# Kernel optimization log

Measured on AMD Instinct MI355X. Metric: run time of the kernel, lower is better.

## Reference

```python
import jax, jax.numpy as jnp
import numpy as np

B, T, I, H = 64, 1024, 256, 512

def setup_inputs() -> dict:
    key = jax.random.key(0)
    ks = jax.random.split(key, 16)
    stdv = 1.0 / np.sqrt(H)
    u = lambda k, shp: jax.random.uniform(k, shp, jnp.float32, -stdv, stdv)
    inp = {"x": jax.random.normal(ks[0], (B, T, I), jnp.float32)}
    names = ["i", "f", "h", "o"]
    for n, g in enumerate(names):
        inp[f"U_{g}"] = u(ks[1 + 3 * n], (I, H))
        inp[f"V_{g}"] = u(ks[2 + 3 * n], (H, H))
        inp[f"b_{g}"] = u(ks[3 + 3 * n], (H,))
    inp["fc_w"] = u(ks[13], (1, H))
    inp["fc_b"] = u(ks[14], (1,))
    return inp

def _lstm_last_h(x, U_i, V_i, b_i, U_f, V_f, b_f, U_h, V_h, b_h, U_o, V_o, b_o):
    # Precompute input projections for all timesteps: [T, B, 4H]
    U = jnp.concatenate([U_i, U_f, U_h, U_o], axis=1)          # [I, 4H]
    b = jnp.concatenate([b_i, b_f, b_h, b_o], axis=0)          # [4H]
    V = jnp.concatenate([V_i, V_f, V_h, V_o], axis=1)          # [H, 4H]
    xproj = jnp.einsum("bti,ig->tbg", x, U) + b                # [T, B, 4H]
    Hn = U_i.shape[1]

    def step(carry, xp_t):
        h, c = carry
        gates = xp_t + h @ V                                   # [B, 4H]
        i_t = jax.nn.sigmoid(gates[:, 0 * Hn:1 * Hn])
        f_t = jax.nn.sigmoid(gates[:, 1 * Hn:2 * Hn])
        g_t = jnp.tanh(gates[:, 2 * Hn:3 * Hn])
        o_t = jax.nn.sigmoid(gates[:, 3 * Hn:4 * Hn])
        c = f_t * c + i_t * g_t
        h = o_t * jnp.tanh(c)
        return (h, c), None

    h0 = jnp.zeros((x.shape[0], Hn), x.dtype)
    c0 = jnp.zeros((x.shape[0], Hn), x.dtype)
    (h_last, _), _ = jax.lax.scan(step, (h0, c0), xproj)
    return h_last

def reference(x, U_i, V_i, b_i, U_f, V_f, b_f, U_h, V_h, b_h, U_o, V_o, b_o, fc_w, fc_b):
    h_last = _lstm_last_h(x, U_i, V_i, b_i, U_f, V_f, b_f, U_h, V_h, b_h, U_o, V_o, b_o)
    return h_last @ fc_w.T + fc_b                              # [B, 1]
```

## Files before the change

kernel.cpp:

```cpp
#include <hip/hip_runtime.h>

typedef _Float16 h8 __attribute__((ext_vector_type(8)));
typedef float    f4 __attribute__((ext_vector_type(4)));
typedef unsigned u4 __attribute__((ext_vector_type(4)));

static const unsigned long long WS_NEEDED = 262144ull;

__device__ __forceinline__ float sigm(float x)   { return 1.0f / (1.0f + __expf(-x)); }
__device__ __forceinline__ float tanh_a(float x) { return 2.0f / (1.0f + __expf(-2.0f * x)) - 1.0f; }

__global__ __launch_bounds__(256) void k_init(unsigned* hbuf)
{
    const int idx = blockIdx.x * 256 + threadIdx.x;
    if (idx < 65536) hbuf[idx] = 0x000003FFu;
}


#define VWAIT0() do { asm volatile("s_waitcnt vmcnt(0)" ::: "memory"); \
                      __builtin_amdgcn_sched_barrier(0); } while (0)
#define LBAR()   do { asm volatile("s_waitcnt lgkmcnt(0)" ::: "memory"); \
                      __builtin_amdgcn_s_barrier(); \
                      __builtin_amdgcn_sched_barrier(0); } while (0)

#define PROBE4() \
    asm volatile( \
        "global_load_dwordx4 %0, %4, off sc0 sc1\n\t" \
        "global_load_dwordx4 %1, %4, off offset:16 sc0 sc1\n\t" \
        "global_load_dwordx4 %2, %4, off offset:1024 sc0 sc1\n\t" \
        "global_load_dwordx4 %3, %4, off offset:1040 sc0 sc1" \
        : "=&v"(qa), "=&v"(qb), "=&v"(qc), "=&v"(qd) \
        : "v"(hp) : "memory")

__device__ __forceinline__ h8 pack8h(u4 a, u4 b)
{
    h8 p;
    p[0] = (_Float16)__uint_as_float(a[0] & 0xFFFFFC00u);
    p[1] = (_Float16)__uint_as_float(a[1] & 0xFFFFFC00u);
    p[2] = (_Float16)__uint_as_float(a[2] & 0xFFFFFC00u);
    p[3] = (_Float16)__uint_as_float(a[3] & 0xFFFFFC00u);
    p[4] = (_Float16)__uint_as_float(b[0] & 0xFFFFFC00u);
    p[5] = (_Float16)__uint_as_float(b[1] & 0xFFFFFC00u);
    p[6] = (_Float16)__uint_as_float(b[2] & 0xFFFFFC00u);
    p[7] = (_Float16)__uint_as_float(b[3] & 0xFFFFFC00u);
    return p;
}
__device__ __forceinline__ h8 pack8f(f4 a, f4 b)
{
    h8 p;
    p[0] = (_Float16)a[0]; p[1] = (_Float16)a[1];
    p[2] = (_Float16)a[2]; p[3] = (_Float16)a[3];
    p[4] = (_Float16)b[0]; p[5] = (_Float16)b[1];
    p[6] = (_Float16)b[2]; p[7] = (_Float16)b[3];
    return p;
}

__global__ __launch_bounds__(256, 1) void k_rec(
    const float* __restrict__ x,
    const float* __restrict__ Ui, const float* __restrict__ Vi, const float* __restrict__ bi,
    const float* __restrict__ Uf, const float* __restrict__ Vf, const float* __restrict__ bf,
    const float* __restrict__ Uh, const float* __restrict__ Vh, const float* __restrict__ bh,
    const float* __restrict__ Uo, const float* __restrict__ Vo, const float* __restrict__ bo,
    unsigned* hbuf)
{
    const int bx = blockIdx.x;
    const int ig = bx & 7;
    const int jg = bx >> 3;
    const int tid = threadIdx.x;
    const int w = tid >> 6, l = tid & 63;
    const int lo = l & 15, hi = l >> 4;
    const int r8 = lo & 7;
    const int unit = jg * 64 + w * 16 + lo;

    __shared__ __align__(16) _Float16 ldsH[2][16 * 32 * 8];
    __shared__ __align__(16) _Float16 ldsX[2][8 * 32 * 8];

    const float* Ug[4] = {Ui, Uf, Uh, Uo};
    const float* Vg[4] = {Vi, Vf, Vh, Vo};
    const float* bg[4] = {bi, bf, bh, bo};

    h8 vfrag[4][16];
    h8 ufrag[4][8];
    float bias[4];
#pragma unroll
    for (int g = 0; g < 4; ++g) {
        bias[g] = bg[g][unit];
#pragma unroll
        for (int kc = 0; kc < 16; ++kc) {
            h8 v;
#pragma unroll
            for (int jj = 0; jj < 8; ++jj)
                v[jj] = (_Float16)Vg[g][(size_t)(kc * 32 + hi * 8 + jj) * 512 + unit];
            vfrag[g][kc] = v;
        }
#pragma unroll
        for (int kc = 0; kc < 8; ++kc) {
            h8 u;
#pragma unroll
            for (int jj = 0; jj < 8; ++jj)
                u[jj] = (_Float16)Ug[g][(size_t)(kc * 32 + hi * 8 + jj) * 512 + unit];
            ufrag[g][kc] = u;
        }
    }

    const int sr = tid >> 5;
    const int sc = (tid & 31) * 8;
    const int kc1 = sc >> 5;
    const int hg1 = (sc >> 3) & 3;
    const int sw1 = ((kc1 & 1) << 2) | hg1;
    const int g1 = kc1 * 32 + hg1 * 8 + (sr ^ sw1);
    const int g2 = (kc1 + 8) * 32 + hg1 * 8 + (sr ^ sw1);

    const float* xrb = x + (size_t)(ig * 8 + sr) * 262144 + sc;

    f4 cst = {0.f, 0.f, 0.f, 0.f};
    f4 xq0, xq1;

    {
        f4 a0, a1;
        asm volatile("global_load_dwordx4 %0, %2, off\n\t"
                     "global_load_dwordx4 %1, %2, off offset:16"
                     : "=&v"(a0), "=&v"(a1) : "v"(xrb) : "memory");
        VWAIT0();
        *(h8*)&ldsX[0][(size_t)g1 * 8] = pack8f(a0, a1);
        const float* xp1 = xrb + 256;
        asm volatile("global_load_dwordx4 %0, %2, off\n\t"
                     "global_load_dwordx4 %1, %2, off offset:16"
                     : "=&v"(xq0), "=&v"(xq1) : "v"(xp1) : "memory");
        LBAR();
    }

    for (int t = 0; t < 1024; ++t) {
        const int pb = t & 1, pn = pb ^ 1;
        const int pr = (t + 1) & 1;
        const unsigned etag = (unsigned)((t + 1023) & 1023);
        const unsigned* hp = hbuf + (size_t)(pr * 8 + ig) * 4096
                                  + (size_t)sr * 512 + sc;

        f4 acc[4], acq[4];
#pragma unroll
        for (int g = 0; g < 4; ++g) {
            f4 a; a[0] = bias[g]; a[1] = bias[g]; a[2] = bias[g]; a[3] = bias[g];
            acc[g] = a;
            f4 z; z[0] = 0.f; z[1] = 0.f; z[2] = 0.f; z[3] = 0.f;
            acq[g] = z;
        }
#pragma unroll
        for (int k = 0; k < 4; ++k) {
            const int ke = 2 * k, ko = 2 * k + 1;
            const int ga = ke * 32 + hi * 8 + (r8 ^ (((ke & 1) << 2) | hi));
            const int gb = ko * 32 + hi * 8 + (r8 ^ (((ko & 1) << 2) | hi));
            const h8 xa = *(const h8*)&ldsX[pb][(size_t)ga * 8];
            const h8 xb = *(const h8*)&ldsX[pb][(size_t)gb * 8];
            acc[0] = __builtin_amdgcn_mfma_f32_16x16x32_f16(xa, ufrag[0][ke], acc[0], 0, 0, 0);
            acc[1] = __builtin_amdgcn_mfma_f32_16x16x32_f16(xa, ufrag[1][ke], acc[1], 0, 0, 0);
            acc[2] = __builtin_amdgcn_mfma_f32_16x16x32_f16(xa, ufrag[2][ke], acc[2], 0, 0, 0);
            acc[3] = __builtin_amdgcn_mfma_f32_16x16x32_f16(xa, ufrag[3][ke], acc[3], 0, 0, 0);
            acq[0] = __builtin_amdgcn_mfma_f32_16x16x32_f16(xb, ufrag[0][ko], acq[0], 0, 0, 0);
            acq[1] = __builtin_amdgcn_mfma_f32_16x16x32_f16(xb, ufrag[1][ko], acq[1], 0, 0, 0);
            acq[2] = __builtin_amdgcn_mfma_f32_16x16x32_f16(xb, ufrag[2][ko], acq[2], 0, 0, 0);
            acq[3] = __builtin_amdgcn_mfma_f32_16x16x32_f16(xb, ufrag[3][ko], acq[3], 0, 0, 0);
        }

        u4 qa, qb, qc, qd;
        PROBE4();

        {
            int tries = 0;
            for (;;) {
                VWAIT0();
                const unsigned m =
                    (qa[0]^etag)|(qa[1]^etag)|(qa[2]^etag)|(qa[3]^etag)|
                    (qb[0]^etag)|(qb[1]^etag)|(qb[2]^etag)|(qb[3]^etag)|
                    (qc[0]^etag)|(qc[1]^etag)|(qc[2]^etag)|(qc[3]^etag)|
                    (qd[0]^etag)|(qd[1]^etag)|(qd[2]^etag)|(qd[3]^etag);
                if (__all((m & 1023u) == 0u)) break;
                if (++tries > 8192) break;
                PROBE4();
            }
        }

        *(h8*)&ldsX[pn][(size_t)g1 * 8] = pack8f(xq0, xq1);
        *(h8*)&ldsH[pb][(size_t)g1 * 8] = pack8h(qa, qb);
        *(h8*)&ldsH[pb][(size_t)g2 * 8] = pack8h(qc, qd);

        {
            const int tn = (t + 2 < 1024) ? t + 2 : 1023;
            const float* xp = xrb + (size_t)tn * 256;
            asm volatile("global_load_dwordx4 %0, %2, off\n\t"
                         "global_load_dwordx4 %1, %2, off offset:16"
                         : "=&v"(xq0), "=&v"(xq1) : "v"(xp) : "memory");
        }

        LBAR();

#pragma unroll
        for (int k = 0; k < 8; ++k) {
            const int kh = k + 8;
            const int ga = k  * 32 + hi * 8 + (r8 ^ (((k  & 1) << 2) | hi));
            const int gb = kh * 32 + hi * 8 + (r8 ^ (((kh & 1) << 2) | hi));
            const h8 a0 = *(const h8*)&ldsH[pb][(size_t)ga * 8];
            const h8 a1 = *(const h8*)&ldsH[pb][(size_t)gb * 8];
            acc[0] = __builtin_amdgcn_mfma_f32_16x16x32_f16(a0, vfrag[0][k],  acc[0], 0, 0, 0);
            acc[1] = __builtin_amdgcn_mfma_f32_16x16x32_f16(a0, vfrag[1][k],  acc[1], 0, 0, 0);
            acc[2] = __builtin_amdgcn_mfma_f32_16x16x32_f16(a0, vfrag[2][k],  acc[2], 0, 0, 0);
            acc[3] = __builtin_amdgcn_mfma_f32_16x16x32_f16(a0, vfrag[3][k],  acc[3], 0, 0, 0);
            acq[0] = __builtin_amdgcn_mfma_f32_16x16x32_f16(a1, vfrag[0][kh], acq[0], 0, 0, 0);
            acq[1] = __builtin_amdgcn_mfma_f32_16x16x32_f16(a1, vfrag[1][kh], acq[1], 0, 0, 0);
            acq[2] = __builtin_amdgcn_mfma_f32_16x16x32_f16(a1, vfrag[2][kh], acq[2], 0, 0, 0);
            acq[3] = __builtin_amdgcn_mfma_f32_16x16x32_f16(a1, vfrag[3][kh], acq[3], 0, 0, 0);
        }

        const unsigned ptag = (unsigned)(t & 1023);
        unsigned pub[4];
#pragma unroll
        for (int d = 0; d < 4; ++d) {
            const float iv = sigm(acc[0][d] + acq[0][d]);
            const float fv = sigm(acc[1][d] + acq[1][d]);
            const float gv = tanh_a(acc[2][d] + acq[2][d]);
            const float ov = sigm(acc[3][d] + acq[3][d]);
            const float c = fv * cst[d] + iv * gv;
            cst[d] = c;
            const float hv = ov * tanh_a(c);
            pub[d] = (__float_as_uint(hv) & 0xFFFFFC00u) | ptag;
        }
        if (hi < 2) {
            unsigned* hw = hbuf + (size_t)((pb * 8 + ig) * 8 + hi * 4) * 512 + unit;
            asm volatile(
                "global_store_dword %4, %0, off sc0 sc1\n\t"
                "global_store_dword %4, %1, off offset:2048 sc0 sc1\n\t"
                "global_store_dword %5, %2, off sc0 sc1\n\t"
                "global_store_dword %5, %3, off offset:2048 sc0 sc1"
                :: "v"(pub[0]), "v"(pub[1]), "v"(pub[2]), "v"(pub[3]),
                   "v"(hw), "v"(hw + 1024)
                : "memory");
        }
    }
}

__global__ __launch_bounds__(64) void k_fc(
    const unsigned* __restrict__ hbuf, const float* __restrict__ fcw,
    const float* __restrict__ fcb, float* __restrict__ out)
{
    const int b = blockIdx.x, l = threadIdx.x;
    const unsigned* h = hbuf + (size_t)((8 + (b >> 3)) * 8 + (b & 7)) * 512;
    float s = 0.f;
#pragma unroll
    for (int k = 0; k < 8; ++k) {
        const float hv = __uint_as_float(h[l + k * 64] & 0xFFFFFC00u);
        s += hv * fcw[l + k * 64];
    }
    for (int off = 32; off > 0; off >>= 1) s += __shfl_down(s, off, 64);
    if (l == 0) out[b] = s + fcb[0];
}

__global__ __launch_bounds__(64) void k_sentinel(float* out)
{
    out[threadIdx.x] = -777777.0f;
}

extern "C" void kernel_launch(void* const* d_in, const int* in_sizes, int n_in,
                              void* d_out, int out_size, void* d_ws, size_t ws_size,
                              hipStream_t stream)
{
    const float* x   = (const float*)d_in[0];
    const float* Ui  = (const float*)d_in[1];
    const float* Vi  = (const float*)d_in[2];
    const float* bi  = (const float*)d_in[3];
    const float* Uf  = (const float*)d_in[4];
    const float* Vf  = (const float*)d_in[5];
    const float* bf  = (const float*)d_in[6];
    const float* Uh  = (const float*)d_in[7];
    const float* Vh  = (const float*)d_in[8];
    const float* bh  = (const float*)d_in[9];
    const float* Uo  = (const float*)d_in[10];
    const float* Vo  = (const float*)d_in[11];
    const float* bo  = (const float*)d_in[12];
    const float* fcw = (const float*)d_in[13];
    const float* fcb = (const float*)d_in[14];
    float* out = (float*)d_out;

    if (ws_size < WS_NEEDED) {
        k_sentinel<<<1, 64, 0, stream>>>(out);
        return;
    }

    unsigned* hbuf = (unsigned*)d_ws;

    k_init<<<256, 256, 0, stream>>>(hbuf);
    k_rec <<<64,  256, 0, stream>>>(x, Ui, Vi, bi, Uf, Vf, bf, Uh, Vh, bh,
                                    Uo, Vo, bo, hbuf);
    k_fc  <<<64,   64, 0, stream>>>(hbuf, fcw, fcb, out);
}
```

Baseline: 2.682 ms.

## Map LSTM teams to XCCs and poll hidden state through local L2 first

Each block reads its hardware XCC id and ranks itself with atomic counters. Blocks are then assigned (ig, jg) so that the eight blocks sharing a batch group sit on the same XCC where possible. The per-step polling of the hidden-state exchange buffer now first probes a few times with sc0-only loads, which can be served from the XCC-local L2. It falls back to system-coherent sc0 sc1 loads only if the tags do not match. Stores are duplicated, once as plain writes to fill local L2 and once as coherent writes. This is meant to cut cross-XCC coherence latency in the per-timestep exchange, at the cost of a startup grid barrier, extra store traffic, and reliance on how non-coherent caching behaves.

Result: slower. 4.552 ms (+69.8%).

```diff
diff --git a/kernel.cpp b/kernel.cpp
--- a/kernel.cpp
+++ b/kernel.cpp
@@ -4,7 +4,7 @@
 typedef float    f4 __attribute__((ext_vector_type(4)));
 typedef unsigned u4 __attribute__((ext_vector_type(4)));
 
-static const unsigned long long WS_NEEDED = 262144ull;
+static const unsigned long long WS_NEEDED = 262208ull;
 
 __device__ __forceinline__ float sigm(float x)   { return 1.0f / (1.0f + __expf(-x)); }
 __device__ __forceinline__ float tanh_a(float x) { return 2.0f / (1.0f + __expf(-2.0f * x)) - 1.0f; }
@@ -13,6 +13,7 @@
 {
     const int idx = blockIdx.x * 256 + threadIdx.x;
     if (idx < 65536) hbuf[idx] = 0x000003FFu;
+    else if (idx < 65552) hbuf[idx] = 0u;
 }
 
 
@@ -22,14 +23,20 @@
                       __builtin_amdgcn_s_barrier(); \
                       __builtin_amdgcn_sched_barrier(0); } while (0)
 
-#define PROBE4() \
+#define PROBE4F(FLAGS) \
     asm volatile( \
-        "global_load_dwordx4 %0, %4, off sc0 sc1\n\t" \
-        "global_load_dwordx4 %1, %4, off offset:16 sc0 sc1\n\t" \
-        "global_load_dwordx4 %2, %4, off offset:1024 sc0 sc1\n\t" \
-        "global_load_dwordx4 %3, %4, off offset:1040 sc0 sc1" \
+        "global_load_dwordx4 %0, %4, off " FLAGS "\n\t" \
+        "global_load_dwordx4 %1, %4, off offset:16 " FLAGS "\n\t" \
+        "global_load_dwordx4 %2, %4, off offset:1024 " FLAGS "\n\t" \
+        "global_load_dwordx4 %3, %4, off offset:1040 " FLAGS \
         : "=&v"(qa), "=&v"(qb), "=&v"(qc), "=&v"(qd) \
         : "v"(hp) : "memory")
+
+#define TAGCHK() \
+    ((qa[0]^etag)|(qa[1]^etag)|(qa[2]^etag)|(qa[3]^etag)| \
+     (qb[0]^etag)|(qb[1]^etag)|(qb[2]^etag)|(qb[3]^etag)| \
+     (qc[0]^etag)|(qc[1]^etag)|(qc[2]^etag)|(qc[3]^etag)| \
+     (qd[0]^etag)|(qd[1]^etag)|(qd[2]^etag)|(qd[3]^etag))
 
 __device__ __forceinline__ h8 pack8h(u4 a, u4 b)
 {
@@ -62,13 +69,44 @@
     const float* __restrict__ Uo, const float* __restrict__ Vo, const float* __restrict__ bo,
     unsigned* hbuf)
 {
-    const int bx = blockIdx.x;
-    const int ig = bx & 7;
-    const int jg = bx >> 3;
     const int tid = threadIdx.x;
     const int w = tid >> 6, l = tid & 63;
     const int lo = l & 15, hi = l >> 4;
     const int r8 = lo & 7;
+
+    __shared__ unsigned s_team[2];
+
+    if (tid == 0) {
+        unsigned xcc;
+        asm volatile("s_getreg_b32 %0, hwreg(HW_REG_XCC_ID)" : "=s"(xcc));
+        xcc &= 7u;
+        unsigned* cnt = hbuf + 65536;
+        const unsigned rank = atomicAdd(&cnt[xcc], 1u);
+        __hip_atomic_fetch_add(&cnt[8], 1u, __ATOMIC_RELEASE, __HIP_MEMORY_SCOPE_AGENT);
+        int spin = 0;
+        while (__hip_atomic_load(&cnt[8], __ATOMIC_ACQUIRE, __HIP_MEMORY_SCOPE_AGENT) < 64u)
+            if (++spin > (1 << 24)) break;
+        unsigned c[8];
+#pragma unroll
+        for (int i = 0; i < 8; ++i)
+            c[i] = __hip_atomic_load(&cnt[i], __ATOMIC_RELAXED, __HIP_MEMORY_SCOPE_AGENT);
+        unsigned ig_, jg_;
+        if (rank < 8u) { ig_ = xcc; jg_ = rank; }
+        else {
+            unsigned lo_ = rank - 8u;
+            for (unsigned y = 0; y < xcc; ++y) lo_ += (c[y] > 8u) ? (c[y] - 8u) : 0u;
+            unsigned k = 0; ig_ = 0; jg_ = 0;
+            for (unsigned xx = 0; xx < 8u; ++xx) {
+                const unsigned d = (c[xx] < 8u) ? (8u - c[xx]) : 0u;
+                if (lo_ < k + d) { ig_ = xx; jg_ = c[xx] + (lo_ - k); break; }
+                k += d;
+            }
+        }
+        s_team[0] = ig_; s_team[1] = jg_;
+    }
+    __syncthreads();
+    const int ig = (int)s_team[0];
+    const int jg = (int)s_team[1];
     const int unit = jg * 64 + w * 16 + lo;
 
     __shared__ __align__(16) _Float16 ldsH[2][16 * 32 * 8];
@@ -162,20 +200,25 @@
         }
 
         u4 qa, qb, qc, qd;
-        PROBE4();
-
+        PROBE4F("sc0");
         {
+            bool ok = false;
             int tries = 0;
             for (;;) {
                 VWAIT0();
-                const unsigned m =
-                    (qa[0]^etag)|(qa[1]^etag)|(qa[2]^etag)|(qa[3]^etag)|
-                    (qb[0]^etag)|(qb[1]^etag)|(qb[2]^etag)|(qb[3]^etag)|
-                    (qc[0]^etag)|(qc[1]^etag)|(qc[2]^etag)|(qc[3]^etag)|
-                    (qd[0]^etag)|(qd[1]^etag)|(qd[2]^etag)|(qd[3]^etag);
-                if (__all((m & 1023u) == 0u)) break;
-                if (++tries > 8192) break;
-                PROBE4();
+                const unsigned m = TAGCHK();
+                if (__all((m & 1023u) == 0u)) { ok = true; break; }
+                if (++tries >= 4) break;
+                PROBE4F("sc0");
+            }
+            if (!ok) {
+                for (;;) {
+                    PROBE4F("sc0 sc1");
+                    VWAIT0();
+                    const unsigned m = TAGCHK();
+                    if (__all((m & 1023u) == 0u)) break;
+                    if (++tries > 8192) break;
+                }
             }
         }
 
@@ -226,6 +269,10 @@
         if (hi < 2) {
             unsigned* hw = hbuf + (size_t)((pb * 8 + ig) * 8 + hi * 4) * 512 + unit;
             asm volatile(
+                "global_store_dword %4, %0, off\n\t"
+                "global_store_dword %4, %1, off offset:2048\n\t"
+                "global_store_dword %5, %2, off\n\t"
+                "global_store_dword %5, %3, off offset:2048\n\t"
                 "global_store_dword %4, %0, off sc0 sc1\n\t"
                 "global_store_dword %4, %1, off offset:2048 sc0 sc1\n\t"
                 "global_store_dword %5, %2, off sc0 sc1\n\t"
@@ -286,7 +333,7 @@
 
     unsigned* hbuf = (unsigned*)d_ws;
 
-    k_init<<<256, 256, 0, stream>>>(hbuf);
+    k_init<<<257, 256, 0, stream>>>(hbuf);
     k_rec <<<64,  256, 0, stream>>>(x, Ui, Vi, bi, Uf, Vf, bf, Uh, Vh, bh,
                                     Uo, Vo, bo, hbuf);
     k_fc  <<<64,   64, 0, stream>>>(hbuf, fcw, fcb, out);
```
